# Performance work log

Hardware: AMD Instinct MI355X
Metric: run time of the kernel (lower is better)

The kernel has to match this reference:

```python
import jax, jax.numpy as jnp
import numpy as np

USER_NUM, ITEM_NUM, D, E, B = 50000, 20000, 64, 2_000_000, 16384
N = USER_NUM + ITEM_NUM


def setup_inputs() -> dict:
    key = jax.random.key(0)
    ks = jax.random.split(key, 20)
    return {
        "user_emb": jax.random.normal(ks[0], (USER_NUM, D), jnp.float32),
        "item_emb": jax.random.normal(ks[1], (ITEM_NUM, D), jnp.float32),
        "edge_row": jax.random.randint(ks[2], (E,), 0, N, jnp.int32),
        "edge_col": jax.random.randint(ks[3], (E,), 0, N, jnp.int32),
        "edge_val": jax.random.uniform(ks[4], (E,), jnp.float32),
        "Wg1": jax.random.normal(ks[5], (D, D), jnp.float32) * 0.05,
        "bg1": jax.random.normal(ks[6], (D,), jnp.float32) * 0.05,
        "Wg2": jax.random.normal(ks[7], (D, D), jnp.float32) * 0.05,
        "bg2": jax.random.normal(ks[8], (D,), jnp.float32) * 0.05,
        "W1": jax.random.normal(ks[9], (4 * D, D), jnp.float32) * 0.05,
        "b1": jax.random.normal(ks[10], (D,), jnp.float32) * 0.05,
        "W2": jax.random.normal(ks[11], (D, 32), jnp.float32) * 0.05,
        "b2": jax.random.normal(ks[12], (32,), jnp.float32) * 0.05,
        "W3": jax.random.normal(ks[13], (32, 1), jnp.float32) * 0.05,
        "b3": jax.random.normal(ks[14], (1,), jnp.float32) * 0.05,
        "userID": jax.random.randint(ks[15], (B,), 0, USER_NUM, jnp.int32),
        "itemID": jax.random.randint(ks[16], (B,), 0, ITEM_NUM, jnp.int32),
    }


def _spmm(row, col, val, x):
    # sparse [N,N] @ dense [N,D] via gather + segment_sum
    msgs = val[:, None] * x[col]  # [E, D]
    return jax.ops.segment_sum(msgs, row, num_segments=N)


def reference(user_emb, item_emb, edge_row, edge_col, edge_val,
              Wg1, bg1, Wg2, bg2, W1, b1, W2, b2, W3, b3, userID, itemID):
    features = jnp.concatenate([user_emb, item_emb], axis=0)  # [N, D]
    final = features
    # single GCN layer (layers=[64,64]); L1 = L + I so SpMM(L1,x) = SpMM(L,x) + x
    lx = _spmm(edge_row, edge_col, edge_val, features)
    lx2 = _spmm(edge_row, edge_col, edge_val, features * features)
    inter1 = (lx + features) @ Wg1 + bg1
    inter2 = lx2 @ Wg2 + bg2
    h = jax.nn.leaky_relu(inter1 + inter2, negative_slope=0.01)
    final = jnp.concatenate([final, h], axis=1)  # [N, 2D]

    u = final[userID]                     # [B, 2D]
    i = final[itemID + USER_NUM]          # [B, 2D]
    embed = jnp.concatenate([u, i], axis=1)  # [B, 4D]
    embed = jax.nn.relu(embed @ W1 + b1)
    embed = jax.nn.relu(embed @ W2 + b2)
    embed = embed @ W3 + b3
    return embed.reshape(-1)
```

## Files before the change

kernel.cpp:

```cpp
#include <hip/hip_runtime.h>
#include <hip/hip_bf16.h>

#define USER_NUM 50000
#define ITEM_NUM 20000
#define NNODE    70000
#define DD       64
#define CHUNK    1024
#define NCHUNK   ((NNODE + CHUNK - 1) / CHUNK)
#define GROWS    (NNODE / 8)
#define APB      2048
#define EPT      8
#define NS2      128
#define NB3      16
#define T_CAP    32768
#define NCHUNK2  (T_CAP / CHUNK)
#define GCAP     327680
#define RT       16

__device__ __forceinline__ const float* feat_row(const float* __restrict__ ue,
                                                 const float* __restrict__ ie, int n) {
    return (n < USER_NUM) ? (ue + (size_t)n * DD)
                          : (ie + (size_t)(n - USER_NUM) * DD);
}


__global__ __launch_bounds__(256) void zero_kernel(int* __restrict__ cnt2,
                                                   int* __restrict__ tmask,
                                                   int* __restrict__ gcur) {
    const int tid    = blockIdx.x * 256 + (int)threadIdx.x;
    const int stride = gridDim.x * 256;
    for (int i = tid; i < T_CAP; i += stride) cnt2[i] = 0;
    for (int i = tid; i < NNODE; i += stride) tmask[i] = 0;
    if (tid < 8) gcur[tid] = tid * GCAP;
}


__global__ __launch_bounds__(256) void mark_kernel(const int* __restrict__ uid,
                                                   const int* __restrict__ iid,
                                                   int* __restrict__ tmask, int B) {
    const int stride = gridDim.x * blockDim.x;
    for (int s = blockIdx.x * blockDim.x + threadIdx.x; s < B; s += stride) {
        tmask[uid[s]] = 1;
        tmask[USER_NUM + iid[s]] = 1;
    }
}


__global__ __launch_bounds__(256) void chunksum_kernel(const int* __restrict__ arr,
                                                       int* __restrict__ csum, int N) {
    __shared__ int red[4];
    const int c = blockIdx.x;
    const int t = threadIdx.x;
    int s = 0;
#pragma unroll
    for (int i = 0; i < 4; ++i) {
        const int idx = c * CHUNK + t + 256 * i;
        s += (idx < N) ? arr[idx] : 0;
    }
#pragma unroll
    for (int off = 32; off; off >>= 1) s += __shfl_down(s, off);
    if ((t & 63) == 0) red[t >> 6] = s;
    __syncthreads();
    if (t == 0) csum[c] = red[0] + red[1] + red[2] + red[3];
}

__global__ __launch_bounds__(128) void scan_small_kernel(const int* __restrict__ csum,
                                                         int* __restrict__ coff,
                                                         int NC) {
    __shared__ int s[128];
    const int t = threadIdx.x;
    const int v = (t < NC) ? csum[t] : 0;
    s[t] = v;
    __syncthreads();
    for (int off = 1; off < 128; off <<= 1) {
        const int val = s[t];
        const int add = (t >= off) ? s[t - off] : 0;
        __syncthreads();
        s[t] = val + add;
        __syncthreads();
    }
    if (t < NC) coff[t] = s[t] - v;
}

__global__ __launch_bounds__(256) void fill_flags_kernel(
    const int* __restrict__ tmask, const int* __restrict__ coff,
    int* __restrict__ cmapx, int* __restrict__ nodes, int* __restrict__ meta,
    int* __restrict__ gslot) {
    __shared__ int sp[256];
    const int c  = blockIdx.x;
    const int t  = threadIdx.x;
    const int g0 = c * CHUNK + t * 4;
    int v[4];
#pragma unroll
    for (int i = 0; i < 4; ++i) v[i] = (g0 + i < NNODE) ? tmask[g0 + i] : 0;
    const int s = ((v[0] + v[1]) + (v[2] + v[3]));
    sp[t] = s;
    __syncthreads();
    for (int off = 1; off < 256; off <<= 1) {
        const int val = sp[t];
        const int add = (t >= off) ? sp[t - off] : 0;
        __syncthreads();
        sp[t] = val + add;
        __syncthreads();
    }
    int run = coff[c] + sp[t] - s;
#pragma unroll
    for (int i = 0; i < 4; ++i) {
        const int g = g0 + i;
        if (g < NNODE) {
            cmapx[g] = v[i] ? run : -1;
            if (v[i]) nodes[run] = g;
            if (g == USER_NUM) meta[1] = run;
            if (g % GROWS == 0) gslot[g / GROWS] = run;
            run += v[i];
        } else if (g == NNODE) {
            meta[0] = run;
            gslot[8] = run;
        }
    }
    if (g0 + 4 == NNODE) { meta[0] = run; gslot[8] = run; }
}

__global__ __launch_bounds__(256) void fill_kernel(const int* __restrict__ cnt,
                                                   const int* __restrict__ coff,
                                                   int* __restrict__ base,
                                                   int* __restrict__ cursor, int N) {
    __shared__ int sp[256];
    const int c  = blockIdx.x;
    const int t  = threadIdx.x;
    const int g0 = c * CHUNK + t * 4;
    int v[4];
#pragma unroll
    for (int i = 0; i < 4; ++i) v[i] = (g0 + i < N) ? cnt[g0 + i] : 0;
    const int s = ((v[0] + v[1]) + (v[2] + v[3]));
    sp[t] = s;
    __syncthreads();
    for (int off = 1; off < 256; off <<= 1) {
        const int val = sp[t];
        const int add = (t >= off) ? sp[t - off] : 0;
        __syncthreads();
        sp[t] = val + add;
        __syncthreads();
    }
    int run = coff[c] + sp[t] - s;
#pragma unroll
    for (int i = 0; i < 4; ++i) {
        const int g = g0 + i;
        if (g < N) {
            base[g]   = run;
            cursor[g] = run;
            run += v[i];
        }
    }
    if (g0 + 4 == N) base[N] = run;
}


__global__ __launch_bounds__(256) void append_kernel(
    const int* __restrict__ erow, const int* __restrict__ ecol,
    const float* __restrict__ eval, const int* __restrict__ cmapx,
    int* __restrict__ gcur, int* __restrict__ grow, int2* __restrict__ gpair,
    int E) {
    __shared__ int lcnt[8];
    __shared__ int lbase[8];
    const int t = threadIdx.x;
    if (t < 8) lcnt[t] = 0;
    __syncthreads();
    const int e0 = blockIdx.x * APB + t;
    int sl[EPT], c[EPT], gr[EPT], rk[EPT];
    float v[EPT];
#pragma unroll
    for (int i = 0; i < EPT; ++i) {
        const int e = e0 + 256 * i;
        gr[i] = -1;
        if (e < E) {
            const int r = erow[e];
            const int slot = cmapx[r];
            if (slot >= 0) {
                sl[i] = slot;
                c[i]  = ecol[e];
                v[i]  = eval[e];
                gr[i] = (r * 8) / NNODE;
                rk[i] = atomicAdd(&lcnt[gr[i]], 1);
            }
        }
    }
    __syncthreads();
    if (t < 8 && lcnt[t] > 0) lbase[t] = atomicAdd(&gcur[t], lcnt[t]);
    __syncthreads();
#pragma unroll
    for (int i = 0; i < EPT; ++i) {
        if (gr[i] >= 0) {
            const int pos = lbase[gr[i]] + rk[i];
            grow[pos]  = sl[i];
            gpair[pos] = make_int2(c[i], __float_as_int(v[i]));
        }
    }
}


__global__ __launch_bounds__(256) void hist3_kernel(const int* __restrict__ grow,
                                                    const int* __restrict__ gcur,
                                                    const int* __restrict__ gslot,
                                                    int* __restrict__ cnt2) {
    __shared__ int hloc[GROWS];
    const int g    = blockIdx.x & 7;
    const int rank = blockIdx.x >> 3;
    const int slo  = gslot[g];
    const int span = gslot[g + 1] - slo;
    for (int i = threadIdx.x; i < span; i += 256) hloc[i] = 0;
    __syncthreads();
    const int hi = gcur[g];
    for (int i = g * GCAP + rank * 256 + (int)threadIdx.x; i < hi; i += NB3 * 256)
        atomicAdd(&hloc[grow[i] - slo], 1);
    __syncthreads();
    for (int i = threadIdx.x; i < span; i += 256) {
        const int v = hloc[i];
        if (v) atomicAdd(&cnt2[slo + i], v);
    }
}


__global__ __launch_bounds__(256) void scatter2_kernel(
    const int* __restrict__ grow, const int2* __restrict__ gpair,
    const int* __restrict__ gcur, int* __restrict__ cursor2,
    int2* __restrict__ epair) {
    const int g    = blockIdx.x & 7;
    const int rank = blockIdx.x >> 3;
    const int hi = gcur[g];
    for (int i = g * GCAP + rank * 256 + (int)threadIdx.x; i < hi; i += NS2 * 256) {
        const int slot = grow[i];
        const int pos = atomicAdd(&cursor2[slot], 1);
        epair[pos] = gpair[i];
    }
}


__global__ __launch_bounds__(256) void spmm_kernel(
    const float* __restrict__ ue, const float* __restrict__ ie,
    const int2* __restrict__ epair, const int* __restrict__ base2,
    const int* __restrict__ nodes, const int* __restrict__ meta,
    float* __restrict__ lx, float* __restrict__ lx2) {
    const int T = meta[0];
    const int lane = threadIdx.x & 63;
    int wv = (int)((blockIdx.x * blockDim.x + threadIdx.x) >> 6);
    wv = __builtin_amdgcn_readfirstlane(wv);
    const int nw = (int)((gridDim.x * blockDim.x) >> 6);
    for (int r = wv; r < T; r += nw) {
        const int jb = base2[r];
        const int je = base2[r + 1];
        float acc1 = 0.f, acc2 = 0.f;
        int j = jb;
        for (; j + 8 <= je; j += 8) {
            int2 p[8];
#pragma unroll
            for (int t = 0; t < 8; ++t) p[t] = epair[j + t];
            float f[8];
#pragma unroll
            for (int t = 0; t < 8; ++t) f[t] = feat_row(ue, ie, p[t].x)[lane];
#pragma unroll
            for (int t = 0; t < 8; ++t) {
                const float v = __int_as_float(p[t].y);
                acc1 = fmaf(v, f[t], acc1);
                acc2 = fmaf(v * f[t], f[t], acc2);
            }
        }
        for (; j + 4 <= je; j += 4) {
            int2 p[4];
#pragma unroll
            for (int t = 0; t < 4; ++t) p[t] = epair[j + t];
            float f[4];
#pragma unroll
            for (int t = 0; t < 4; ++t) f[t] = feat_row(ue, ie, p[t].x)[lane];
#pragma unroll
            for (int t = 0; t < 4; ++t) {
                const float v = __int_as_float(p[t].y);
                acc1 = fmaf(v, f[t], acc1);
                acc2 = fmaf(v * f[t], f[t], acc2);
            }
        }
        for (; j < je; ++j) {
            const int2 p = epair[j];
            const float f = feat_row(ue, ie, p.x)[lane];
            const float v = __int_as_float(p.y);
            acc1 = fmaf(v, f, acc1);
            acc2 = fmaf(v * f, f, acc2);
        }
        const int n = nodes[r];
        lx [(size_t)r * DD + lane] = acc1 + feat_row(ue, ie, n)[lane];
        lx2[(size_t)r * DD + lane] = acc2;
    }
}


__global__ __launch_bounds__(256) void xform_fused_kernel(
    const float* __restrict__ lx, const float* __restrict__ lx2,
    const float* __restrict__ ue, const float* __restrict__ ie,
    const float* __restrict__ Wg1, const float* __restrict__ Wg2,
    const float* __restrict__ bg1, const float* __restrict__ bg2,
    const float* __restrict__ W1, const float* __restrict__ b1,
    float* __restrict__ part,
    const int* __restrict__ nodes, const int* __restrict__ meta, int nTilesU) {
    const int Tu = meta[1];
    const int T  = meta[0];
    const bool isU   = (int)blockIdx.x < nTilesU;
    const int tileIx = isU ? blockIdx.x : (blockIdx.x - nTilesU);
    const int start  = isU ? 0  : Tu;
    const int lim    = isU ? Tu : T;
    const int tb     = start + tileIx * RT;
    if (tb >= lim) return;
    const float* fb = isU ? ue : ie;

    __shared__ float sH[RT * DD];
    __shared__ float sP[RT * DD];
    const int t     = threadIdx.x;
    const int lane  = t & 63;
    const int w     = t >> 6;
    const int khalf = (w & 1) * 32;
    const int rhalf = (w >> 1) * (RT / 2);

    float wva[32], wvb[32];
#pragma unroll
    for (int k = 0; k < 32; ++k) {
        wva[k] = Wg1[(khalf + k) * DD + lane];
        wvb[k] = Wg2[(khalf + k) * DD + lane];
    }

    float4* sHv = (float4*)sH;
    float4* sPv = (float4*)sP;
    sPv[t] = make_float4(0.f, 0.f, 0.f, 0.f);
    __syncthreads();

#pragma unroll 2
    for (int r = 0; r < RT / 2; ++r) {
        const int row = rhalf + r;
        int gc = min(tb + row, lim - 1);
        gc = __builtin_amdgcn_readfirstlane(gc);
        const float* xr = lx  + (size_t)gc * DD + khalf;
        const float* yr = lx2 + (size_t)gc * DD + khalf;
        float o0 = 0.f, o1 = 0.f, o2 = 0.f, o3 = 0.f;
#pragma unroll
        for (int q = 0; q < 8; ++q) {
            o0 = fmaf(xr[4 * q + 0], wva[4 * q + 0], o0);
            o1 = fmaf(xr[4 * q + 1], wva[4 * q + 1], o1);
            o0 = fmaf(xr[4 * q + 2], wva[4 * q + 2], o0);
            o1 = fmaf(xr[4 * q + 3], wva[4 * q + 3], o1);
            o2 = fmaf(yr[4 * q + 0], wvb[4 * q + 0], o2);
            o3 = fmaf(yr[4 * q + 1], wvb[4 * q + 1], o3);
            o2 = fmaf(yr[4 * q + 2], wvb[4 * q + 2], o2);
            o3 = fmaf(yr[4 * q + 3], wvb[4 * q + 3], o3);
        }
        atomicAdd(&sP[row * DD + lane], (o0 + o1) + (o2 + o3));
    }
    __syncthreads();

    {
        const int c = t & 15;
        float4 v = sPv[t];
        const float4 ba = ((const float4*)bg1)[c];
        const float4 bb = ((const float4*)bg2)[c];
        v.x += ba.x + bb.x; v.y += ba.y + bb.y;
        v.z += ba.z + bb.z; v.w += ba.w + bb.w;
        v.x = (v.x > 0.f) ? v.x : 0.01f * v.x;
        v.y = (v.y > 0.f) ? v.y : 0.01f * v.y;
        v.z = (v.z > 0.f) ? v.z : 0.01f * v.z;
        v.w = (v.w > 0.f) ? v.w : 0.01f * v.w;
        sHv[t] = v;
        sPv[t] = make_float4(0.f, 0.f, 0.f, 0.f);
    }

    const float* W1a = W1 + (isU ? 0 : 2 * DD * DD);
    const float* W1b = W1a + DD * DD;
#pragma unroll
    for (int k = 0; k < 32; ++k) {
        wva[k] = W1b[(khalf + k) * DD + lane];
        wvb[k] = W1a[(khalf + k) * DD + lane];
    }
    __syncthreads();

#pragma unroll 2
    for (int r = 0; r < RT / 2; ++r) {
        const int row = rhalf + r;
        int gc = min(tb + row, lim - 1);
        gc = __builtin_amdgcn_readfirstlane(gc);
        int n = nodes[gc];
        if (!isU) n -= USER_NUM;
        n = __builtin_amdgcn_readfirstlane(n);
        const float* fr = fb + (size_t)n * DD + khalf;
        const float* hr = &sH[row * DD + khalf];
        float o0 = 0.f, o1 = 0.f, o2 = 0.f, o3 = 0.f;
#pragma unroll
        for (int q = 0; q < 8; ++q) {
            const float4 qh = *(const float4*)(hr + 4 * q);
            o0 = fmaf(qh.x, wva[4 * q + 0], o0);
            o1 = fmaf(qh.y, wva[4 * q + 1], o1);
            o0 = fmaf(qh.z, wva[4 * q + 2], o0);
            o1 = fmaf(qh.w, wva[4 * q + 3], o1);
            o2 = fmaf(fr[4 * q + 0], wvb[4 * q + 0], o2);
            o3 = fmaf(fr[4 * q + 1], wvb[4 * q + 1], o3);
            o2 = fmaf(fr[4 * q + 2], wvb[4 * q + 2], o2);
            o3 = fmaf(fr[4 * q + 3], wvb[4 * q + 3], o3);
        }
        atomicAdd(&sP[row * DD + lane], (o0 + o1) + (o2 + o3));
    }
    __syncthreads();

    {
        const int row = t >> 4;
        const int c   = t & 15;
        const int g   = tb + row;
        float4 v = sPv[t];
        if (isU) {
            const float4 b = ((const float4*)b1)[c];
            v.x += b.x; v.y += b.y; v.z += b.z; v.w += b.w;
        }
        if (g < lim) ((float4*)part)[(size_t)g * 16 + c] = v;
    }
}


__global__ __launch_bounds__(256) void mlp_kernel(
    const float* __restrict__ part, const int* __restrict__ cmapx,
    const float* __restrict__ W2, const float* __restrict__ b2,
    const float* __restrict__ W3, const float* __restrict__ b3,
    const int* __restrict__ uid, const int* __restrict__ iid,
    float* __restrict__ out, int B) {
    __shared__ float sW2[DD * 32];
    __shared__ float sW3[32];
    for (int i = threadIdx.x; i < DD * 32; i += 256) sW2[i] = W2[i];
    if (threadIdx.x < 32) sW3[threadIdx.x] = W3[threadIdx.x];
    __syncthreads();
    const int lane = threadIdx.x & 63;
    const int wave = (int)((blockIdx.x * blockDim.x + threadIdx.x) >> 6);
    const int nw   = (int)((gridDim.x * blockDim.x) >> 6);
    const float bias2 = b2[lane & 31];
    const float w3v   = sW3[lane & 31];
    const float bias3 = b3[0];
    for (int s = wave; s < B; s += nw) {
        const int su = cmapx[uid[s]];
        const int si = cmapx[USER_NUM + iid[s]];
        const float pu = part[(size_t)su * DD + lane];
        const float pi = part[(size_t)si * DD + lane];
        const float x  = pu + pi;
        const float o1 = (x > 0.f) ? x : 0.f;
        float acc_a = bias2, acc_b = 0.f;
#pragma unroll
        for (int k = 0; k < DD; k += 2) {
            acc_a = fmaf(__shfl(o1, k),     sW2[k * 32 + (lane & 31)],       acc_a);
            acc_b = fmaf(__shfl(o1, k + 1), sW2[(k + 1) * 32 + (lane & 31)], acc_b);
        }
        const float a2 = acc_a + acc_b;
        const float o2 = (a2 > 0.f) ? a2 : 0.f;
        float p = o2 * w3v;
        p += __shfl_xor(p, 1);
        p += __shfl_xor(p, 2);
        p += __shfl_xor(p, 4);
        p += __shfl_xor(p, 8);
        p += __shfl_xor(p, 16);
        if (lane == 0) out[s] = p + bias3;
    }
}

extern "C" void kernel_launch(void* const* d_in, const int* in_sizes, int n_in,
                              void* d_out, int out_size, void* d_ws, size_t ws_size,
                              hipStream_t stream) {
    const float* ue   = (const float*)d_in[0];
    const float* ie   = (const float*)d_in[1];
    const int*   erow = (const int*)d_in[2];
    const int*   ecol = (const int*)d_in[3];
    const float* evalp= (const float*)d_in[4];
    const float* Wg1  = (const float*)d_in[5];
    const float* bg1  = (const float*)d_in[6];
    const float* Wg2  = (const float*)d_in[7];
    const float* bg2  = (const float*)d_in[8];
    const float* W1   = (const float*)d_in[9];
    const float* b1   = (const float*)d_in[10];
    const float* W2   = (const float*)d_in[11];
    const float* b2   = (const float*)d_in[12];
    const float* W3   = (const float*)d_in[13];
    const float* b3   = (const float*)d_in[14];
    const int*   uid  = (const int*)d_in[15];
    const int*   iid  = (const int*)d_in[16];
    float* out = (float*)d_out;

    const int E = in_sizes[2];
    const int B = in_sizes[15];

    const int TU_MAX = (B < USER_NUM) ? B : USER_NUM;
    const int TI_MAX = (B < ITEM_NUM) ? B : ITEM_NUM;
    const int nTilesU = (TU_MAX + RT - 1) / RT;
    const int nTilesI = (TI_MAX + RT - 1) / RT;

    char* ws = (char*)d_ws;
    const size_t ndc = (size_t)T_CAP * DD;
    float* lx    = (float*)ws;
    float* lx2   = lx + ndc;
    float* part  = lx2 + ndc;
    int*   grow  = (int*)ws;
    int2*  gpair = (int2*)(ws + 11u * 1024 * 1024);
    char*  tail  = ws + 32u * 1024 * 1024;
    int2*  epair = (int2*)tail;
    int*   mi    = (int*)(tail + (size_t)E * sizeof(int2));
    int*   cnt2    = mi;
    int*   cursor2 = cnt2 + T_CAP;
    int*   base2   = cursor2 + T_CAP;
    int*   tmask   = base2 + T_CAP + 1;
    int*   cmapx   = tmask + NNODE;
    int*   nodes   = cmapx + NNODE;
    int*   csum    = nodes + T_CAP;
    int*   coff    = csum + 128;
    int*   gcur    = coff + 128;
    int*   meta    = gcur + 8;
    int*   gslot   = meta + 8;

    zero_kernel<<<512, 256, 0, stream>>>(cnt2, tmask, gcur);
    mark_kernel<<<(B + 255) / 256, 256, 0, stream>>>(uid, iid, tmask, B);
    chunksum_kernel<<<NCHUNK, 256, 0, stream>>>(tmask, csum, NNODE);
    scan_small_kernel<<<1, 128, 0, stream>>>(csum, coff, NCHUNK);
    fill_flags_kernel<<<NCHUNK, 256, 0, stream>>>(tmask, coff, cmapx, nodes,
                                                  meta, gslot);
    append_kernel<<<(E + APB - 1) / APB, 256, 0, stream>>>(
        erow, ecol, evalp, cmapx, gcur, grow, gpair, E);
    hist3_kernel<<<8 * NB3, 256, 0, stream>>>(grow, gcur, gslot, cnt2);
    chunksum_kernel<<<NCHUNK2, 256, 0, stream>>>(cnt2, csum, T_CAP);
    scan_small_kernel<<<1, 128, 0, stream>>>(csum, coff, NCHUNK2);
    fill_kernel<<<NCHUNK2, 256, 0, stream>>>(cnt2, coff, base2, cursor2, T_CAP);
    scatter2_kernel<<<8 * NS2, 256, 0, stream>>>(grow, gpair, gcur, cursor2, epair);
    spmm_kernel<<<4096, 256, 0, stream>>>(ue, ie, epair, base2, nodes, meta,
                                          lx, lx2);

    xform_fused_kernel<<<nTilesU + nTilesI, 256, 0, stream>>>(
        lx, lx2, ue, ie, Wg1, Wg2, bg1, bg2, W1, b1, part, nodes, meta, nTilesU);

    mlp_kernel<<<1024, 256, 0, stream>>>(part, cmapx, W2, b2, W3, b3,
                                         uid, iid, out, B);
}
```

Baseline: 197.6 us.

## Make xform kernel grid-stride with weights held in registers across tiles

The fused transform kernel becomes persistent: a fixed grid of 344 user blocks and 168 item blocks loops over 16-row tiles instead of launching one block per tile. All four 32-wide weight slices (Wg1, Wg2, W1 halves) and the biases are loaded into registers once per block and reused across every tile. This cuts repeated per-tile weight reloads and block launches. The cost is about 128 live weight registers per thread, which may reduce occupancy, plus an extra barrier per tile.

```diff
diff --git a/kernel.cpp b/kernel.cpp
--- a/kernel.cpp
+++ b/kernel.cpp
@@ -16,6 +16,8 @@
 #define NCHUNK2  (T_CAP / CHUNK)
 #define GCAP     327680
 #define RT       16
+#define XGU      344
+#define XGI      168
 
 __device__ __forceinline__ const float* feat_row(const float* __restrict__ ue,
                                                  const float* __restrict__ ie, int n) {
@@ -293,23 +295,26 @@
 }
 
 
-__global__ __launch_bounds__(256) void xform_fused_kernel(
+__global__ __launch_bounds__(256) void xform_gs_kernel(
     const float* __restrict__ lx, const float* __restrict__ lx2,
     const float* __restrict__ ue, const float* __restrict__ ie,
     const float* __restrict__ Wg1, const float* __restrict__ Wg2,
     const float* __restrict__ bg1, const float* __restrict__ bg2,
     const float* __restrict__ W1, const float* __restrict__ b1,
     float* __restrict__ part,
-    const int* __restrict__ nodes, const int* __restrict__ meta, int nTilesU) {
+    const int* __restrict__ nodes, const int* __restrict__ meta) {
     const int Tu = meta[1];
     const int T  = meta[0];
-    const bool isU   = (int)blockIdx.x < nTilesU;
-    const int tileIx = isU ? blockIdx.x : (blockIdx.x - nTilesU);
-    const int start  = isU ? 0  : Tu;
-    const int lim    = isU ? Tu : T;
-    const int tb     = start + tileIx * RT;
-    if (tb >= lim) return;
-    const float* fb = isU ? ue : ie;
+    const bool isU  = (int)blockIdx.x < XGU;
+    const int rank  = isU ? blockIdx.x : (blockIdx.x - XGU);
+    const int nBlk  = isU ? XGU : XGI;
+    const int start = isU ? 0 : Tu;
+    const int count = isU ? Tu : (T - Tu);
+    const int nTiles = (count + RT - 1) / RT;
+    const int lim   = start + count;
+    const float* fb  = isU ? ue : ie;
+    const float* W1a = W1 + (isU ? 0 : 2 * DD * DD);
+    const float* W1b = W1a + DD * DD;
 
     __shared__ float sH[RT * DD];
     __shared__ float sP[RT * DD];
@@ -319,11 +324,21 @@
     const int khalf = (w & 1) * 32;
     const int rhalf = (w >> 1) * (RT / 2);
 
-    float wva[32], wvb[32];
+    float wg_a[32], wg_b[32], w1_h[32], w1_f[32];
 #pragma unroll
     for (int k = 0; k < 32; ++k) {
-        wva[k] = Wg1[(khalf + k) * DD + lane];
-        wvb[k] = Wg2[(khalf + k) * DD + lane];
+        wg_a[k] = Wg1[(khalf + k) * DD + lane];
+        wg_b[k] = Wg2[(khalf + k) * DD + lane];
+        w1_h[k] = W1b[(khalf + k) * DD + lane];
+        w1_f[k] = W1a[(khalf + k) * DD + lane];
+    }
+    const int ec = t & 15;
+    float4 bgv, b1v;
+    {
+        const float4 a = ((const float4*)bg1)[ec];
+        const float4 b = ((const float4*)bg2)[ec];
+        bgv = make_float4(a.x + b.x, a.y + b.y, a.z + b.z, a.w + b.w);
+        b1v = isU ? ((const float4*)b1)[ec] : make_float4(0.f, 0.f, 0.f, 0.f);
     }
 
     float4* sHv = (float4*)sH;
@@ -331,90 +346,80 @@
     sPv[t] = make_float4(0.f, 0.f, 0.f, 0.f);
     __syncthreads();
 
+    for (int tile = rank; tile < nTiles; tile += nBlk) {
+        const int tb = start + tile * RT;
+
 #pragma unroll 2
-    for (int r = 0; r < RT / 2; ++r) {
-        const int row = rhalf + r;
-        int gc = min(tb + row, lim - 1);
-        gc = __builtin_amdgcn_readfirstlane(gc);
-        const float* xr = lx  + (size_t)gc * DD + khalf;
-        const float* yr = lx2 + (size_t)gc * DD + khalf;
-        float o0 = 0.f, o1 = 0.f, o2 = 0.f, o3 = 0.f;
-#pragma unroll
-        for (int q = 0; q < 8; ++q) {
-            o0 = fmaf(xr[4 * q + 0], wva[4 * q + 0], o0);
-            o1 = fmaf(xr[4 * q + 1], wva[4 * q + 1], o1);
-            o0 = fmaf(xr[4 * q + 2], wva[4 * q + 2], o0);
-            o1 = fmaf(xr[4 * q + 3], wva[4 * q + 3], o1);
-            o2 = fmaf(yr[4 * q + 0], wvb[4 * q + 0], o2);
-            o3 = fmaf(yr[4 * q + 1], wvb[4 * q + 1], o3);
-            o2 = fmaf(yr[4 * q + 2], wvb[4 * q + 2], o2);
-            o3 = fmaf(yr[4 * q + 3], wvb[4 * q + 3], o3);
-        }
-        atomicAdd(&sP[row * DD + lane], (o0 + o1) + (o2 + o3));
-    }
-    __syncthreads();
-
-    {
-        const int c = t & 15;
-        float4 v = sPv[t];
-        const float4 ba = ((const float4*)bg1)[c];
-        const float4 bb = ((const float4*)bg2)[c];
-        v.x += ba.x + bb.x; v.y += ba.y + bb.y;
-        v.z += ba.z + bb.z; v.w += ba.w + bb.w;
-        v.x = (v.x > 0.f) ? v.x : 0.01f * v.x;
-        v.y = (v.y > 0.f) ? v.y : 0.01f * v.y;
-        v.z = (v.z > 0.f) ? v.z : 0.01f * v.z;
-        v.w = (v.w > 0.f) ? v.w : 0.01f * v.w;
-        sHv[t] = v;
-        sPv[t] = make_float4(0.f, 0.f, 0.f, 0.f);
-    }
-
-    const float* W1a = W1 + (isU ? 0 : 2 * DD * DD);
-    const float* W1b = W1a + DD * DD;
-#pragma unroll
-    for (int k = 0; k < 32; ++k) {
-        wva[k] = W1b[(khalf + k) * DD + lane];
-        wvb[k] = W1a[(khalf + k) * DD + lane];
-    }
-    __syncthreads();
+        for (int r = 0; r < RT / 2; ++r) {
+            const int row = rhalf + r;
+            int gc = min(tb + row, lim - 1);
+            gc = __builtin_amdgcn_readfirstlane(gc);
+            const float* xr = lx  + (size_t)gc * DD + khalf;
+            const float* yr = lx2 + (size_t)gc * DD + khalf;
+            float o0 = 0.f, o1 = 0.f, o2 = 0.f, o3 = 0.f;
+#pragma unroll
+            for (int q = 0; q < 8; ++q) {
+                o0 = fmaf(xr[4 * q + 0], wg_a[4 * q + 0], o0);
+                o1 = fmaf(xr[4 * q + 1], wg_a[4 * q + 1], o1);
+                o0 = fmaf(xr[4 * q + 2], wg_a[4 * q + 2], o0);
+                o1 = fmaf(xr[4 * q + 3], wg_a[4 * q + 3], o1);
+                o2 = fmaf(yr[4 * q + 0], wg_b[4 * q + 0], o2);
+                o3 = fmaf(yr[4 * q + 1], wg_b[4 * q + 1], o3);
+                o2 = fmaf(yr[4 * q + 2], wg_b[4 * q + 2], o2);
+                o3 = fmaf(yr[4 * q + 3], wg_b[4 * q + 3], o3);
+            }
+            atomicAdd(&sP[row * DD + lane], (o0 + o1) + (o2 + o3));
+        }
+        __syncthreads();
+
+        {
+            float4 v = sPv[t];
+            v.x += bgv.x; v.y += bgv.y; v.z += bgv.z; v.w += bgv.w;
+            v.x = (v.x > 0.f) ? v.x : 0.01f * v.x;
+            v.y = (v.y > 0.f) ? v.y : 0.01f * v.y;
+            v.z = (v.z > 0.f) ? v.z : 0.01f * v.z;
+            v.w = (v.w > 0.f) ? v.w : 0.01f * v.w;
+            sHv[t] = v;
+            sPv[t] = make_float4(0.f, 0.f, 0.f, 0.f);
+        }
+        __syncthreads();
 
 #pragma unroll 2
-    for (int r = 0; r < RT / 2; ++r) {
-        const int row = rhalf + r;
-        int gc = min(tb + row, lim - 1);
-        gc = __builtin_amdgcn_readfirstlane(gc);
-        int n = nodes[gc];
-        if (!isU) n -= USER_NUM;
-        n = __builtin_amdgcn_readfirstlane(n);
-        const float* fr = fb + (size_t)n * DD + khalf;
-        const float* hr = &sH[row * DD + khalf];
-        float o0 = 0.f, o1 = 0.f, o2 = 0.f, o3 = 0.f;
-#pragma unroll
-        for (int q = 0; q < 8; ++q) {
-            const float4 qh = *(const float4*)(hr + 4 * q);
-            o0 = fmaf(qh.x, wva[4 * q + 0], o0);
-            o1 = fmaf(qh.y, wva[4 * q + 1], o1);
-            o0 = fmaf(qh.z, wva[4 * q + 2], o0);
-            o1 = fmaf(qh.w, wva[4 * q + 3], o1);
-            o2 = fmaf(fr[4 * q + 0], wvb[4 * q + 0], o2);
-            o3 = fmaf(fr[4 * q + 1], wvb[4 * q + 1], o3);
-            o2 = fmaf(fr[4 * q + 2], wvb[4 * q + 2], o2);
-            o3 = fmaf(fr[4 * q + 3], wvb[4 * q + 3], o3);
-        }
-        atomicAdd(&sP[row * DD + lane], (o0 + o1) + (o2 + o3));
-    }
-    __syncthreads();
-
-    {
-        const int row = t >> 4;
-        const int c   = t & 15;
-        const int g   = tb + row;
-        float4 v = sPv[t];
-        if (isU) {
-            const float4 b = ((const float4*)b1)[c];
-            v.x += b.x; v.y += b.y; v.z += b.z; v.w += b.w;
-        }
-        if (g < lim) ((float4*)part)[(size_t)g * 16 + c] = v;
+        for (int r = 0; r < RT / 2; ++r) {
+            const int row = rhalf + r;
+            int gc = min(tb + row, lim - 1);
+            gc = __builtin_amdgcn_readfirstlane(gc);
+            int n = nodes[gc];
+            if (!isU) n -= USER_NUM;
+            n = __builtin_amdgcn_readfirstlane(n);
+            const float* fr = fb + (size_t)n * DD + khalf;
+            const float* hr = &sH[row * DD + khalf];
+            float o0 = 0.f, o1 = 0.f, o2 = 0.f, o3 = 0.f;
+#pragma unroll
+            for (int q = 0; q < 8; ++q) {
+                const float4 qh = *(const float4*)(hr + 4 * q);
+                o0 = fmaf(qh.x, w1_h[4 * q + 0], o0);
+                o1 = fmaf(qh.y, w1_h[4 * q + 1], o1);
+                o0 = fmaf(qh.z, w1_h[4 * q + 2], o0);
+                o1 = fmaf(qh.w, w1_h[4 * q + 3], o1);
+                o2 = fmaf(fr[4 * q + 0], w1_f[4 * q + 0], o2);
+                o3 = fmaf(fr[4 * q + 1], w1_f[4 * q + 1], o3);
+                o2 = fmaf(fr[4 * q + 2], w1_f[4 * q + 2], o2);
+                o3 = fmaf(fr[4 * q + 3], w1_f[4 * q + 3], o3);
+            }
+            atomicAdd(&sP[row * DD + lane], (o0 + o1) + (o2 + o3));
+        }
+        __syncthreads();
+
+        {
+            const int row = t >> 4;
+            const int g   = tb + row;
+            float4 v = sPv[t];
+            v.x += b1v.x; v.y += b1v.y; v.z += b1v.z; v.w += b1v.w;
+            if (g < lim) ((float4*)part)[(size_t)g * 16 + ec] = v;
+            sPv[t] = make_float4(0.f, 0.f, 0.f, 0.f);
+        }
+        __syncthreads();
     }
 }
 
@@ -486,11 +491,6 @@
     const int E = in_sizes[2];
     const int B = in_sizes[15];
 
-    const int TU_MAX = (B < USER_NUM) ? B : USER_NUM;
-    const int TI_MAX = (B < ITEM_NUM) ? B : ITEM_NUM;
-    const int nTilesU = (TU_MAX + RT - 1) / RT;
-    const int nTilesI = (TI_MAX + RT - 1) / RT;
-
     char* ws = (char*)d_ws;
     const size_t ndc = (size_t)T_CAP * DD;
     float* lx    = (float*)ws;
@@ -529,8 +529,8 @@
     spmm_kernel<<<4096, 256, 0, stream>>>(ue, ie, epair, base2, nodes, meta,
                                           lx, lx2);
 
-    xform_fused_kernel<<<nTilesU + nTilesI, 256, 0, stream>>>(
-        lx, lx2, ue, ie, Wg1, Wg2, bg1, bg2, W1, b1, part, nodes, meta, nTilesU);
+    xform_gs_kernel<<<XGU + XGI, 256, 0, stream>>>(
+        lx, lx2, ue, ie, Wg1, Wg2, bg1, bg2, W1, b1, part, nodes, meta);
 
     mlp_kernel<<<1024, 256, 0, stream>>>(part, cmapx, W2, b2, W3, b3,
                                          uid, iid, out, B);
```

New measurement: 209.2 us. +5.9%, slower.

## Replace per-row CSR sort with 64-row bins and LDS-atomic SpMM

Applied to the files above, without the earlier changes.

Drops the histogram, scan, fill and per-row scatter passes that built exact CSR for the active rows. Edges are now re-bucketed into fixed-capacity bins of 64 destination rows. A per-bin SpMM kernel then accumulates lx and lx2 in shared memory with atomics, which cuts several kernel launches and a global counting pass. The price is shared-memory atomic contention and 32KB x2 of LDS per block, which limits occupancy. The fixed bin capacity (BCAP=4032) can overflow when degree is skewed, which would be a silent correctness risk.

```diff
diff --git a/kernel.cpp b/kernel.cpp
--- a/kernel.cpp
+++ b/kernel.cpp
@@ -10,12 +10,14 @@
 #define GROWS    (NNODE / 8)
 #define APB      2048
 #define EPT      8
-#define NS2      128
-#define NB3      16
 #define T_CAP    32768
-#define NCHUNK2  (T_CAP / CHUNK)
 #define GCAP     327680
 #define RT       16
+#define BSLOT    64
+#define NBIN     (T_CAP / BSLOT)
+#define BCAP     4032
+#define NSR      64
+#define MAXBINS  160
 
 __device__ __forceinline__ const float* feat_row(const float* __restrict__ ue,
                                                  const float* __restrict__ ie, int n) {
@@ -24,14 +26,14 @@
 }
 
 
-__global__ __launch_bounds__(256) void zero_kernel(int* __restrict__ cnt2,
-                                                   int* __restrict__ tmask,
-                                                   int* __restrict__ gcur) {
+__global__ __launch_bounds__(256) void zero_kernel(int* __restrict__ tmask,
+                                                   int* __restrict__ gcur,
+                                                   int* __restrict__ bcur) {
     const int tid    = blockIdx.x * 256 + (int)threadIdx.x;
     const int stride = gridDim.x * 256;
-    for (int i = tid; i < T_CAP; i += stride) cnt2[i] = 0;
     for (int i = tid; i < NNODE; i += stride) tmask[i] = 0;
     if (tid < 8) gcur[tid] = tid * GCAP;
+    if (tid < NBIN) bcur[tid] = tid * BCAP;
 }
 
 
@@ -119,40 +121,6 @@
         }
     }
     if (g0 + 4 == NNODE) { meta[0] = run; gslot[8] = run; }
-}
-
-__global__ __launch_bounds__(256) void fill_kernel(const int* __restrict__ cnt,
-                                                   const int* __restrict__ coff,
-                                                   int* __restrict__ base,
-                                                   int* __restrict__ cursor, int N) {
-    __shared__ int sp[256];
-    const int c  = blockIdx.x;
-    const int t  = threadIdx.x;
-    const int g0 = c * CHUNK + t * 4;
-    int v[4];
-#pragma unroll
-    for (int i = 0; i < 4; ++i) v[i] = (g0 + i < N) ? cnt[g0 + i] : 0;
-    const int s = ((v[0] + v[1]) + (v[2] + v[3]));
-    sp[t] = s;
-    __syncthreads();
-    for (int off = 1; off < 256; off <<= 1) {
-        const int val = sp[t];
-        const int add = (t >= off) ? sp[t - off] : 0;
-        __syncthreads();
-        sp[t] = val + add;
-        __syncthreads();
-    }
-    int run = coff[c] + sp[t] - s;
-#pragma unroll
-    for (int i = 0; i < 4; ++i) {
-        const int g = g0 + i;
-        if (g < N) {
-            base[g]   = run;
-            cursor[g] = run;
-            run += v[i];
-        }
-    }
-    if (g0 + 4 == N) base[N] = run;
 }
 
 
@@ -199,96 +167,115 @@
 }
 
 
-__global__ __launch_bounds__(256) void hist3_kernel(const int* __restrict__ grow,
-                                                    const int* __restrict__ gcur,
-                                                    const int* __restrict__ gslot,
-                                                    int* __restrict__ cnt2) {
-    __shared__ int hloc[GROWS];
+__global__ __launch_bounds__(256) void rebin_kernel(
+    const int* __restrict__ grow, const int2* __restrict__ gpair,
+    const int* __restrict__ gcur, const int* __restrict__ gslot,
+    int* __restrict__ bcur, int2* __restrict__ gpair2,
+    unsigned short* __restrict__ srow2) {
+    __shared__ int lcnt[MAXBINS];
+    __shared__ int lbase[MAXBINS];
     const int g    = blockIdx.x & 7;
     const int rank = blockIdx.x >> 3;
-    const int slo  = gslot[g];
-    const int span = gslot[g + 1] - slo;
-    for (int i = threadIdx.x; i < span; i += 256) hloc[i] = 0;
-    __syncthreads();
-    const int hi = gcur[g];
-    for (int i = g * GCAP + rank * 256 + (int)threadIdx.x; i < hi; i += NB3 * 256)
-        atomicAdd(&hloc[grow[i] - slo], 1);
-    __syncthreads();
-    for (int i = threadIdx.x; i < span; i += 256) {
-        const int v = hloc[i];
-        if (v) atomicAdd(&cnt2[slo + i], v);
-    }
-}
-
-
-__global__ __launch_bounds__(256) void scatter2_kernel(
-    const int* __restrict__ grow, const int2* __restrict__ gpair,
-    const int* __restrict__ gcur, int* __restrict__ cursor2,
-    int2* __restrict__ epair) {
-    const int g    = blockIdx.x & 7;
-    const int rank = blockIdx.x >> 3;
-    const int hi = gcur[g];
-    for (int i = g * GCAP + rank * 256 + (int)threadIdx.x; i < hi; i += NS2 * 256) {
-        const int slot = grow[i];
-        const int pos = atomicAdd(&cursor2[slot], 1);
-        epair[pos] = gpair[i];
-    }
-}
-
-
-__global__ __launch_bounds__(256) void spmm_kernel(
+    const int lo_g = g * GCAP;
+    const int hi_g = gcur[g];
+    const int cnt  = hi_g - lo_g;
+    if (cnt <= 0) return;
+    const int CH = (cnt + NSR - 1) / NSR;
+    const int lo = lo_g + rank * CH;
+    const int hi = min(lo + CH, hi_g);
+    if (lo >= hi) return;
+    const int b0 = gslot[g] >> 6;
+    const int nb = ((gslot[g + 1] - 1) >> 6) - b0 + 1;
+
+    for (int w0 = lo; w0 < hi; w0 += 256 * EPT) {
+        for (int i = threadIdx.x; i < nb; i += 256) lcnt[i] = 0;
+        __syncthreads();
+        int sl[EPT], bi[EPT], rk[EPT];
+        int2 pv[EPT];
+#pragma unroll
+        for (int i = 0; i < EPT; ++i) {
+            const int e = w0 + (int)threadIdx.x + 256 * i;
+            bi[i] = -1;
+            if (e < hi) {
+                sl[i] = grow[e];
+                pv[i] = gpair[e];
+                bi[i] = (sl[i] >> 6) - b0;
+                rk[i] = atomicAdd(&lcnt[bi[i]], 1);
+            }
+        }
+        __syncthreads();
+        for (int i = threadIdx.x; i < nb; i += 256)
+            lbase[i] = lcnt[i] ? atomicAdd(&bcur[b0 + i], lcnt[i]) : 0;
+        __syncthreads();
+#pragma unroll
+        for (int i = 0; i < EPT; ++i) {
+            if (bi[i] >= 0) {
+                const int pos = lbase[bi[i]] + rk[i];
+                gpair2[pos] = pv[i];
+                srow2[pos]  = (unsigned short)sl[i];
+            }
+        }
+        __syncthreads();
+    }
+}
+
+
+__global__ __launch_bounds__(256) void bspmm_kernel(
     const float* __restrict__ ue, const float* __restrict__ ie,
-    const int2* __restrict__ epair, const int* __restrict__ base2,
-    const int* __restrict__ nodes, const int* __restrict__ meta,
+    const int2* __restrict__ gpair2, const unsigned short* __restrict__ srow2,
+    const int* __restrict__ bcur, const int* __restrict__ nodes,
+    const int* __restrict__ meta,
     float* __restrict__ lx, float* __restrict__ lx2) {
-    const int T = meta[0];
+    __shared__ float a1[BSLOT * DD];
+    __shared__ float a2[BSLOT * DD];
+    const int bin  = blockIdx.x;
+    const int T    = meta[0];
     const int lane = threadIdx.x & 63;
-    int wv = (int)((blockIdx.x * blockDim.x + threadIdx.x) >> 6);
-    wv = __builtin_amdgcn_readfirstlane(wv);
-    const int nw = (int)((gridDim.x * blockDim.x) >> 6);
-    for (int r = wv; r < T; r += nw) {
-        const int jb = base2[r];
-        const int je = base2[r + 1];
-        float acc1 = 0.f, acc2 = 0.f;
-        int j = jb;
-        for (; j + 8 <= je; j += 8) {
-            int2 p[8];
-#pragma unroll
-            for (int t = 0; t < 8; ++t) p[t] = epair[j + t];
-            float f[8];
-#pragma unroll
-            for (int t = 0; t < 8; ++t) f[t] = feat_row(ue, ie, p[t].x)[lane];
-#pragma unroll
-            for (int t = 0; t < 8; ++t) {
-                const float v = __int_as_float(p[t].y);
-                acc1 = fmaf(v, f[t], acc1);
-                acc2 = fmaf(v * f[t], f[t], acc2);
-            }
-        }
-        for (; j + 4 <= je; j += 4) {
-            int2 p[4];
-#pragma unroll
-            for (int t = 0; t < 4; ++t) p[t] = epair[j + t];
-            float f[4];
-#pragma unroll
-            for (int t = 0; t < 4; ++t) f[t] = feat_row(ue, ie, p[t].x)[lane];
-#pragma unroll
-            for (int t = 0; t < 4; ++t) {
-                const float v = __int_as_float(p[t].y);
-                acc1 = fmaf(v, f[t], acc1);
-                acc2 = fmaf(v * f[t], f[t], acc2);
-            }
-        }
-        for (; j < je; ++j) {
-            const int2 p = epair[j];
-            const float f = feat_row(ue, ie, p.x)[lane];
-            const float v = __int_as_float(p.y);
-            acc1 = fmaf(v, f, acc1);
-            acc2 = fmaf(v * f, f, acc2);
-        }
-        const int n = nodes[r];
-        lx [(size_t)r * DD + lane] = acc1 + feat_row(ue, ie, n)[lane];
-        lx2[(size_t)r * DD + lane] = acc2;
+    const int w    = threadIdx.x >> 6;
+    for (int i = threadIdx.x; i < BSLOT * DD; i += 256) { a1[i] = 0.f; a2[i] = 0.f; }
+    __syncthreads();
+
+    const int lo = bin * BCAP;
+    const int hi = bcur[bin];
+    const int base = bin * BSLOT;
+
+    for (int p = lo + w * 8; p + 8 <= hi; p += 32) {
+        int2 pv[8];
+        int  sr[8];
+#pragma unroll
+        for (int t = 0; t < 8; ++t) { pv[t] = gpair2[p + t]; sr[t] = srow2[p + t]; }
+        float f[8];
+#pragma unroll
+        for (int t = 0; t < 8; ++t) f[t] = feat_row(ue, ie, pv[t].x)[lane];
+#pragma unroll
+        for (int t = 0; t < 8; ++t) {
+            const float v  = __int_as_float(pv[t].y);
+            const int   lr = (sr[t] - base) * DD + lane;
+            atomicAdd(&a1[lr], v * f[t]);
+            atomicAdd(&a2[lr], v * f[t] * f[t]);
+        }
+    }
+    if (w == 0) {
+        const int pend = lo + ((hi - lo) / 8) * 8;
+        for (int e = pend; e < hi; ++e) {
+            const int2 pv = gpair2[e];
+            const int  sr = srow2[e];
+            const float f = feat_row(ue, ie, pv.x)[lane];
+            const float v = __int_as_float(pv.y);
+            const int  lr = (sr - base) * DD + lane;
+            atomicAdd(&a1[lr], v * f);
+            atomicAdd(&a2[lr], v * f * f);
+        }
+    }
+    __syncthreads();
+
+    for (int s = w; s < BSLOT; s += 4) {
+        const int g = base + s;
+        if (g < T) {
+            const int n = nodes[g];
+            lx [(size_t)g * DD + lane] = a1[s * DD + lane] + feat_row(ue, ie, n)[lane];
+            lx2[(size_t)g * DD + lane] = a2[s * DD + lane];
+        }
     }
 }
 
@@ -491,29 +478,27 @@
     const int nTilesU = (TU_MAX + RT - 1) / RT;
     const int nTilesI = (TI_MAX + RT - 1) / RT;
 
+    const size_t MB = 1u << 20;
     char* ws = (char*)d_ws;
-    const size_t ndc = (size_t)T_CAP * DD;
-    float* lx    = (float*)ws;
-    float* lx2   = lx + ndc;
-    float* part  = lx2 + ndc;
-    int*   grow  = (int*)ws;
-    int2*  gpair = (int2*)(ws + 11u * 1024 * 1024);
-    char*  tail  = ws + 32u * 1024 * 1024;
-    int2*  epair = (int2*)tail;
-    int*   mi    = (int*)(tail + (size_t)E * sizeof(int2));
-    int*   cnt2    = mi;
-    int*   cursor2 = cnt2 + T_CAP;
-    int*   base2   = cursor2 + T_CAP;
-    int*   tmask   = base2 + T_CAP + 1;
-    int*   cmapx   = tmask + NNODE;
-    int*   nodes   = cmapx + NNODE;
-    int*   csum    = nodes + T_CAP;
-    int*   coff    = csum + 128;
-    int*   gcur    = coff + 128;
-    int*   meta    = gcur + 8;
-    int*   gslot   = meta + 8;
-
-    zero_kernel<<<512, 256, 0, stream>>>(cnt2, tmask, gcur);
+    float* lx    = (float*)(ws);
+    float* lx2   = (float*)(ws + 8 * MB);
+    float* part  = (float*)(ws + 16 * MB);
+    int*   grow  = (int*)(ws + 24 * MB);
+    int2*  gpair = (int2*)(ws + 36 * MB);
+    int2*  gpair2= (int2*)(ws + 58 * MB);
+    unsigned short* srow2 = (unsigned short*)(ws + 76 * MB);
+    int*   mi    = (int*)(ws + 82 * MB);
+    int*   tmask = mi;
+    int*   cmapx = tmask + NNODE;
+    int*   nodes = cmapx + NNODE;
+    int*   csum  = nodes + T_CAP;
+    int*   coff  = csum + 128;
+    int*   gcur  = coff + 128;
+    int*   bcur  = gcur + 8;
+    int*   meta  = bcur + NBIN;
+    int*   gslot = meta + 8;
+
+    zero_kernel<<<512, 256, 0, stream>>>(tmask, gcur, bcur);
     mark_kernel<<<(B + 255) / 256, 256, 0, stream>>>(uid, iid, tmask, B);
     chunksum_kernel<<<NCHUNK, 256, 0, stream>>>(tmask, csum, NNODE);
     scan_small_kernel<<<1, 128, 0, stream>>>(csum, coff, NCHUNK);
@@ -521,13 +506,10 @@
                                                   meta, gslot);
     append_kernel<<<(E + APB - 1) / APB, 256, 0, stream>>>(
         erow, ecol, evalp, cmapx, gcur, grow, gpair, E);
-    hist3_kernel<<<8 * NB3, 256, 0, stream>>>(grow, gcur, gslot, cnt2);
-    chunksum_kernel<<<NCHUNK2, 256, 0, stream>>>(cnt2, csum, T_CAP);
-    scan_small_kernel<<<1, 128, 0, stream>>>(csum, coff, NCHUNK2);
-    fill_kernel<<<NCHUNK2, 256, 0, stream>>>(cnt2, coff, base2, cursor2, T_CAP);
-    scatter2_kernel<<<8 * NS2, 256, 0, stream>>>(grow, gpair, gcur, cursor2, epair);
-    spmm_kernel<<<4096, 256, 0, stream>>>(ue, ie, epair, base2, nodes, meta,
-                                          lx, lx2);
+    rebin_kernel<<<8 * NSR, 256, 0, stream>>>(grow, gpair, gcur, gslot,
+                                              bcur, gpair2, srow2);
+    bspmm_kernel<<<NBIN, 256, 0, stream>>>(ue, ie, gpair2, srow2, bcur,
+                                           nodes, meta, lx, lx2);
 
     xform_fused_kernel<<<nTilesU + nTilesI, 256, 0, stream>>>(
         lx, lx2, ue, ie, Wg1, Wg2, bg1, bg2, W1, b1, part, nodes, meta, nTilesU);
```

Result: slower. 752.7 us (+280.9%).
